# Performance work log

Hardware: AMD Instinct MI355X
Metric: run time of the kernel (lower is better)

## Reference

```python
import jax, jax.numpy as jnp
import numpy as np

B, S, D, H, DH = 4, 2048, 1024, 16, 64
INIT_STD = 0.02
IGNORE = -100000.0


def setup_inputs() -> dict:
    key = jax.random.key(0)
    ks = jax.random.split(key, 5)
    x = jax.random.normal(ks[0], (B, S, D), dtype=jnp.float32)
    W_Q = INIT_STD * jax.random.normal(ks[1], (H, D, DH), dtype=jnp.float32)
    W_K = INIT_STD * jax.random.normal(ks[2], (H, D, DH), dtype=jnp.float32)
    W_V = INIT_STD * jax.random.normal(ks[3], (H, D, DH), dtype=jnp.float32)
    W_O = INIT_STD * jax.random.normal(ks[4], (H, DH, D), dtype=jnp.float32)
    b_Q = jnp.zeros((H, DH), dtype=jnp.float32)
    b_K = jnp.zeros((H, DH), dtype=jnp.float32)
    b_V = jnp.zeros((H, DH), dtype=jnp.float32)
    b_O = jnp.zeros((D,), dtype=jnp.float32)
    return {"x": x, "W_Q": W_Q, "b_Q": b_Q, "W_K": W_K, "b_K": b_K,
            "W_V": W_V, "b_V": b_V, "W_O": W_O, "b_O": b_O}


def reference(x, W_Q, b_Q, W_K, b_K, W_V, b_V, W_O, b_O):
    # x: (B, S, D); projections -> (B, S, H, DH)
    Q = jnp.einsum('bqd,hde->bqhe', x, W_Q) + b_Q
    K = jnp.einsum('bkd,hde->bkhe', x, W_K) + b_K
    V = jnp.einsum('bkd,hde->bkhe', x, W_V) + b_V
    d_head = Q.shape[-1]
    # scores: (B, H, Sq, Sk)
    scores = jnp.einsum('bqhe,bkhe->bhqk', Q, K) / np.sqrt(d_head).astype(np.float32)
    s = scores.shape[-1]
    causal = jnp.triu(jnp.ones((s, s), dtype=bool), k=1)
    scores = jnp.where(causal, jnp.float32(IGNORE), scores)
    A = jax.nn.softmax(scores, axis=-1)
    z = jnp.einsum('bhqk,bkhe->bqhe', A, V)
    # output projection: sum over heads + bias
    attn_out = jnp.einsum('bqhe,hed->bqd', z, W_O) + b_O
    return attn_out
```

## Files before the change

kernel.cpp:

```cpp
#include <hip/hip_runtime.h>


#define B_ 4
#define S_ 2048
#define D_ 1024
#define H_ 16
#define DH_ 64

typedef unsigned short ushort_t;
typedef __attribute__((ext_vector_type(4))) short short4v;
typedef __attribute__((ext_vector_type(8))) short short8v;
typedef __attribute__((ext_vector_type(4))) float floatx4;
typedef __attribute__((ext_vector_type(4))) unsigned short ushort4v;

static __device__ __forceinline__ ushort_t f2bf(float f) {
    union { float f; unsigned u; } v; v.f = f;
    unsigned r = v.u + 0x7fffu + ((v.u >> 16) & 1u);
    return (ushort_t)(r >> 16);
}

static __device__ __forceinline__ float fast_exp2(float x) {
#if __has_builtin(__builtin_amdgcn_exp2f)
    return __builtin_amdgcn_exp2f(x);
#else
    return exp2f(x);
#endif
}

static __device__ __forceinline__ unsigned pack_bf16_tr(float lo, float hi) {
    union { float f; unsigned u; } a, b;
    a.f = lo; b.f = hi;
    return __builtin_amdgcn_perm(b.u, a.u, 0x07060302u);
}

static __device__ __forceinline__ void g2lds16(const void* g, void* l) {
    __builtin_amdgcn_global_load_lds(
        (__attribute__((address_space(1))) void*)(unsigned long long)(size_t)g,
        (__attribute__((address_space(3))) void*)(unsigned int)(size_t)l,
        16, 0, 0);
}

__global__ void convert_x_kernel(const float* __restrict__ x, ushort_t* __restrict__ xb) {
    int i = (blockIdx.x * 256 + threadIdx.x) * 4;
    float4 v = *(const float4*)&x[i];
    ushort4v o;
    o[0] = f2bf(v.x); o[1] = f2bf(v.y); o[2] = f2bf(v.z); o[3] = f2bf(v.w);
    *(ushort4v*)&xb[i] = o;
}

__global__ void transpose_nk_kernel(const float* __restrict__ s0, const float* __restrict__ s1,
                                    const float* __restrict__ s2, ushort_t* __restrict__ dst,
                                    int mode) {
    __shared__ float tile[32][33];
    int z = blockIdx.z;
    const float* src;
    ushort_t* d;
    int C;
    if (mode == 0) {
        src = (z < 16 ? s0 : (z < 32 ? s1 : s2)) + (size_t)(z & 15) * 65536;
        d = dst + (size_t)z * 65536;
        C = 64;
    } else {
        src = s0 + (size_t)z * 65536;
        d = dst + (size_t)z * 64;
        C = 1024;
    }
    int r0 = blockIdx.x * 32, c0 = blockIdx.y * 32;
    int tx = threadIdx.x, ty = threadIdx.y;
#pragma unroll
    for (int i = 0; i < 4; ++i)
        tile[ty + i * 8][tx] = src[(size_t)(r0 + ty + i * 8) * C + c0 + tx];
    __syncthreads();
#pragma unroll
    for (int i = 0; i < 4; ++i)
        d[(size_t)(c0 + ty + i * 8) * 1024 + r0 + tx] = f2bf(tile[tx][ty + i * 8]);
}

__global__ __launch_bounds__(256) void gemm_qkv(const ushort_t* __restrict__ A,
                                                const ushort_t* __restrict__ Wt,
                                                const float* __restrict__ bq,
                                                const float* __restrict__ bk,
                                                const float* __restrict__ bv,
                                                ushort_t* __restrict__ Qw,
                                                ushort_t* __restrict__ Kw,
                                                ushort_t* __restrict__ Vw) {
    __shared__ ushort_t sA[128 * 64];
    __shared__ ushort_t sB[128 * 64];
    const int tid = threadIdx.x;
    const int lane = tid & 63, w = tid >> 6;
    const int lq = lane & 15, quad = lane >> 4;
    const int wm = w >> 1, wn = w & 1;
    const int m0 = blockIdx.y * 128, n0 = blockIdx.x * 128;
    const int mat = blockIdx.x >> 3;

    floatx4 acc[4][4] = {};

    for (int k0 = 0; k0 < 1024; k0 += 64) {
        __syncthreads();
#pragma unroll
        for (int p = 0; p < 4; ++p) {
            int rr = w * 32 + p * 8 + (lane >> 3);
            int cc = (lane & 7) ^ (rr & 7);
            g2lds16(&A[(size_t)(m0 + rr) * 1024 + k0 + cc * 8], &sA[(w * 32 + p * 8) * 64]);
            g2lds16(&Wt[(size_t)(n0 + rr) * 1024 + k0 + cc * 8], &sB[(w * 32 + p * 8) * 64]);
        }
        __syncthreads();
#pragma unroll
        for (int ks = 0; ks < 2; ++ks) {
            short8v af[4], bfr[4];
#pragma unroll
            for (int t = 0; t < 4; ++t) {
                int ma = wm * 64 + t * 16 + lq;
                af[t] = *(const short8v*)&sA[ma * 64 + ((((ks << 2) | quad) ^ (ma & 7)) << 3)];
                int nb = wn * 64 + t * 16 + lq;
                bfr[t] = *(const short8v*)&sB[nb * 64 + ((((ks << 2) | quad) ^ (nb & 7)) << 3)];
            }
#pragma unroll
            for (int mt = 0; mt < 4; ++mt)
#pragma unroll
                for (int nt = 0; nt < 4; ++nt)
                    acc[mt][nt] = __builtin_amdgcn_mfma_f32_16x16x32_bf16(af[mt], bfr[nt], acc[mt][nt], 0, 0, 0);
        }
    }

    const float* bias = mat == 0 ? bq : (mat == 1 ? bk : bv);
    float bias_v[4];
#pragma unroll
    for (int nt = 0; nt < 4; ++nt) bias_v[nt] = bias[(n0 & 1023) + wn * 64 + nt * 16 + lq];

#pragma unroll
    for (int mt = 0; mt < 4; ++mt) {
#pragma unroll
        for (int nt = 0; nt < 4; ++nt) {
            int row0 = m0 + wm * 64 + mt * 16 + quad * 4;
            int col = (n0 & 1023) + wn * 64 + nt * 16 + lq;
            int h = col >> 6, e = col & 63;
            if (mat == 2) {
                int b = row0 >> 11, s = row0 & 2047;
                ushort4v pk;
#pragma unroll
                for (int rg = 0; rg < 4; ++rg) pk[rg] = f2bf(acc[mt][nt][rg] + bias_v[nt]);
                *(ushort4v*)&Vw[((size_t)((b << 4) | h) * 64 + e) * 2048 + s] = pk;
            } else {
                ushort_t* Du = mat == 0 ? Qw : Kw;
#pragma unroll
                for (int rg = 0; rg < 4; ++rg) {
                    int row = row0 + rg;
                    int b = row >> 11, s = row & 2047;
                    float v = acc[mt][nt][rg] + bias_v[nt];
                    if (mat == 0) v *= 0.18033688011112042f;
                    Du[((size_t)((b << 4) | h) * 2048 + s) * 64 + e] = f2bf(v);
                }
            }
        }
    }
}

#define VROW 132
__global__ __launch_bounds__(256) void attn_kernel(const ushort_t* __restrict__ Q,
                                                   const ushort_t* __restrict__ Kg,
                                                   const ushort_t* __restrict__ Vt,
                                                   ushort_t* __restrict__ Z) {
    __shared__ ushort_t sK[2][128 * 64];
    __shared__ ushort_t sV[64 * VROW];
    const int tid = threadIdx.x;
    const int lane = tid & 63, w = tid >> 6;
    const int lq = lane & 15, quad = lane >> 4;
    const int bh = blockIdx.y;
    const int b = bh >> 4, h = bh & 15;
    const ushort_t* Qp = Q + (size_t)bh * S_ * DH_;
    const ushort_t* Kp = Kg + (size_t)bh * S_ * DH_;
    const ushort_t* Vp = Vt + (size_t)bh * DH_ * S_;

    const int kbase0 = lq * 64 + ((quad ^ (lq & 7)) << 3);
    const int kbase1 = lq * 64 + (((4 | quad) ^ (lq & 7)) << 3);
    const int vbase = lq * VROW + quad * 4;
    const int vr = w * 16 + (lane >> 2);
    const int vc = (lane & 3) * 32;

    const floatx4 fzero = {0.f, 0.f, 0.f, 0.f};

    auto stageK = [&](int kt, int bs) __attribute__((always_inline)) {
        ushort_t* dK = sK[bs];
#pragma unroll
        for (int p = 0; p < 4; ++p) {
            int rrk = w * 32 + p * 8 + (lane >> 3);
            int ck = (lane & 7) ^ (rrk & 7);
            g2lds16(&Kp[(size_t)(kt * 128 + rrk) * 64 + ck * 8], &dK[(w * 32 + p * 8) * 64]);
        }
    };
    auto loadV = [&](int kt, short8v* vr4) __attribute__((always_inline)) {
        const ushort_t* src = &Vp[(size_t)vr * 2048 + kt * 128 + vc];
#pragma unroll
        for (int j = 0; j < 4; ++j) vr4[j] = *(const short8v*)&src[j * 8];
    };
    auto writeV = [&](const short8v* vr4) __attribute__((always_inline)) {
        ushort_t* dst = &sV[vr * VROW + vc];
#pragma unroll
        for (int j = 0; j < 4; ++j) *(short8v*)&dst[j * 8] = vr4[j];
    };

    for (int pass = 0; pass < 2; ++pass) {
        const int qt = pass == 0 ? (int)blockIdx.x : 15 - (int)blockIdx.x;
        const int q0 = qt * 128;

        short8v qf[2][2];
#pragma unroll
        for (int qi = 0; qi < 2; ++qi)
#pragma unroll
            for (int ks = 0; ks < 2; ++ks)
                qf[qi][ks] = *(const short8v*)&Qp[(size_t)(q0 + w * 32 + qi * 16 + lq) * DH_ + ks * 32 + quad * 8];

        float l_i[2] = {0.f, 0.f};
        floatx4 o[2][4] = {};
        short8v vreg[4];

        stageK(0, 0);
        loadV(0, vreg);

        for (int kt = 0; kt <= qt; ++kt) {
            const bool diag = (kt == qt);
            const ushort_t* cK = sK[kt & 1];

            __syncthreads();
            writeV(vreg);
            if (kt < qt) {
                stageK(kt + 1, (kt + 1) & 1);
                loadV(kt + 1, vreg);
            }

            floatx4 st[8][2];
#pragma unroll
            for (int si = 0; si < 8; ++si) {
                short8v a0 = *(const short8v*)&cK[kbase0 + si * 1024];
                short8v a1 = *(const short8v*)&cK[kbase1 + si * 1024];
#pragma unroll
                for (int qi = 0; qi < 2; ++qi) {
                    st[si][qi] = __builtin_amdgcn_mfma_f32_16x16x32_bf16(a0, qf[qi][0], fzero, 0, 0, 0);
                    st[si][qi] = __builtin_amdgcn_mfma_f32_16x16x32_bf16(a1, qf[qi][1], st[si][qi], 0, 0, 0);
                }
            }

            short4v pf[8][2];
#pragma unroll
            for (int qi = 0; qi < 2; ++qi) {
                const int qg = q0 + w * 32 + qi * 16 + lq;
                float lsum = 0.f;
#pragma unroll
                for (int si = 0; si < 8; ++si) {
                    float p[4];
#pragma unroll
                    for (int rg = 0; rg < 4; ++rg) {
                        float v = st[si][qi][rg];
                        if (diag) {
                            int sg = kt * 128 + si * 16 + quad * 4 + rg;
                            if (sg > qg) v = -1e30f;
                        }
                        p[rg] = fast_exp2(v);
                        lsum += p[rg];
                    }
                    union { unsigned u[2]; short4v v4; } pk;
                    pk.u[0] = pack_bf16_tr(p[0], p[1]);
                    pk.u[1] = pack_bf16_tr(p[2], p[3]);
                    pf[si][qi] = pk.v4;
                }
                l_i[qi] += lsum;
            }

            __syncthreads();

#pragma unroll
            for (int ksp = 0; ksp < 8; ++ksp) {
#pragma unroll
                for (int et = 0; et < 4; ++et) {
                    short4v vf = *(const short4v*)&sV[vbase + et * (16 * VROW) + ksp * 16];
#pragma unroll
                    for (int qi = 0; qi < 2; ++qi)
                        o[qi][et] = __builtin_amdgcn_mfma_f32_16x16x16bf16_1k(pf[ksp][qi], vf, o[qi][et], 0, 0, 0);
                }
            }
        }

#pragma unroll
        for (int qi = 0; qi < 2; ++qi) {
            float lf = l_i[qi];
            lf += __shfl_xor(lf, 16);
            lf += __shfl_xor(lf, 32);
            float linv[4];
#pragma unroll
            for (int rg = 0; rg < 4; ++rg) linv[rg] = 1.0f / __shfl(lf, quad * 4 + rg);
#pragma unroll
            for (int et = 0; et < 4; ++et) {
#pragma unroll
                for (int rg = 0; rg < 4; ++rg) {
                    int qg = q0 + w * 32 + qi * 16 + quad * 4 + rg;
                    int e = et * 16 + lq;
                    Z[((size_t)(b * S_ + qg) * H_ + h) * DH_ + e] = f2bf(o[qi][et][rg] * linv[rg]);
                }
            }
        }
    }
}

__global__ __launch_bounds__(256) void gemm_o(const ushort_t* __restrict__ A,
                                              const ushort_t* __restrict__ Bt,
                                              const float* __restrict__ bias,
                                              float* __restrict__ Dst) {
    __shared__ ushort_t sA[128 * 64];
    __shared__ ushort_t sB[128 * 64];
    const int tid = threadIdx.x;
    const int lane = tid & 63, w = tid >> 6;
    const int lq = lane & 15, quad = lane >> 4;
    const int wm = w >> 1, wn = w & 1;
    const int m0 = blockIdx.y * 128, n0 = blockIdx.x * 128;

    floatx4 acc[4][4] = {};

    for (int k0 = 0; k0 < 1024; k0 += 64) {
        __syncthreads();
#pragma unroll
        for (int p = 0; p < 4; ++p) {
            int rr = w * 32 + p * 8 + (lane >> 3);
            int cc = (lane & 7) ^ (rr & 7);
            g2lds16(&A[(size_t)(m0 + rr) * 1024 + k0 + cc * 8], &sA[(w * 32 + p * 8) * 64]);
            g2lds16(&Bt[(size_t)(n0 + rr) * 1024 + k0 + cc * 8], &sB[(w * 32 + p * 8) * 64]);
        }
        __syncthreads();
#pragma unroll
        for (int ks = 0; ks < 2; ++ks) {
            short8v af[4], bfr[4];
#pragma unroll
            for (int t = 0; t < 4; ++t) {
                int ma = wm * 64 + t * 16 + lq;
                af[t] = *(const short8v*)&sA[ma * 64 + ((((ks << 2) | quad) ^ (ma & 7)) << 3)];
                int nb = wn * 64 + t * 16 + lq;
                bfr[t] = *(const short8v*)&sB[nb * 64 + ((((ks << 2) | quad) ^ (nb & 7)) << 3)];
            }
#pragma unroll
            for (int mt = 0; mt < 4; ++mt)
#pragma unroll
                for (int nt = 0; nt < 4; ++nt)
                    acc[mt][nt] = __builtin_amdgcn_mfma_f32_16x16x32_bf16(af[mt], bfr[nt], acc[mt][nt], 0, 0, 0);
        }
    }

    float bias_v[4];
#pragma unroll
    for (int nt = 0; nt < 4; ++nt) bias_v[nt] = bias[n0 + wn * 64 + nt * 16 + lq];

#pragma unroll
    for (int mt = 0; mt < 4; ++mt) {
#pragma unroll
        for (int nt = 0; nt < 4; ++nt) {
            int row0 = m0 + wm * 64 + mt * 16 + quad * 4;
            int col = n0 + wn * 64 + nt * 16 + lq;
#pragma unroll
            for (int rg = 0; rg < 4; ++rg)
                Dst[(size_t)(row0 + rg) * 1024 + col] = acc[mt][nt][rg] + bias_v[nt];
        }
    }
}

extern "C" void kernel_launch(void* const* d_in, const int* in_sizes, int n_in,
                              void* d_out, int out_size, void* d_ws, size_t ws_size,
                              hipStream_t stream) {
    const float* x  = (const float*)d_in[0];
    const float* wq = (const float*)d_in[1];
    const float* bq = (const float*)d_in[2];
    const float* wk = (const float*)d_in[3];
    const float* bk = (const float*)d_in[4];
    const float* wv = (const float*)d_in[5];
    const float* bv = (const float*)d_in[6];
    const float* wo = (const float*)d_in[7];
    const float* bo = (const float*)d_in[8];

    char* ws = (char*)d_ws;
    size_t off = 0;
    ushort_t* xb  = (ushort_t*)(ws + off); off += (size_t)8192 * 1024 * 2;
    ushort_t* wt  = (ushort_t*)(ws + off); off += (size_t)3 * 1024 * 1024 * 2;
    ushort_t* wot = (ushort_t*)(ws + off); off += (size_t)1024 * 1024 * 2;
    ushort_t* Qw  = (ushort_t*)(ws + off); off += (size_t)8192 * 1024 * 2;
    ushort_t* Kw  = (ushort_t*)(ws + off); off += (size_t)8192 * 1024 * 2;
    ushort_t* Vw  = (ushort_t*)(ws + off); off += (size_t)8192 * 1024 * 2;
    ushort_t* Zw  = (ushort_t*)(ws + off); off += (size_t)8192 * 1024 * 2;

    convert_x_kernel<<<8192, 256, 0, stream>>>(x, xb);
    transpose_nk_kernel<<<dim3(32, 2, 48), dim3(32, 8), 0, stream>>>(wq, wk, wv, wt, 0);
    transpose_nk_kernel<<<dim3(2, 32, 16), dim3(32, 8), 0, stream>>>(wo, nullptr, nullptr, wot, 1);
    gemm_qkv<<<dim3(24, 64), 256, 0, stream>>>(xb, wt, bq, bk, bv, Qw, Kw, Vw);
    attn_kernel<<<dim3(8, 64), 256, 0, stream>>>(Qw, Kw, Vw, Zw);
    gemm_o<<<dim3(8, 64), 256, 0, stream>>>(Zw, wot, bo, (float*)d_out);
}
```

Measured before the change: 268.5 us.

## Merge prep kernels into one launch and swap grid axes for block ordering

Folds the x conversion and both weight-transpose kernels into a single prep launch, removing two kernel launches. It swaps the grid dimensions in the QKV GEMM, attention and output GEMM so that consecutive blocks walk along M (or batch-head) rather than N, which changes L2 reuse of the weight and activation tiles across concurrently scheduled blocks. It also changes the V LDS row padding from 132 to 140 to alter the bank-conflict pattern. The reordering could help or hurt cache locality, and the merged prep kernel adds a branch on block index.

```diff
diff --git a/kernel.cpp b/kernel.cpp
--- a/kernel.cpp
+++ b/kernel.cpp
@@ -40,33 +40,39 @@
         16, 0, 0);
 }
 
-__global__ void convert_x_kernel(const float* __restrict__ x, ushort_t* __restrict__ xb) {
-    int i = (blockIdx.x * 256 + threadIdx.x) * 4;
-    float4 v = *(const float4*)&x[i];
-    ushort4v o;
-    o[0] = f2bf(v.x); o[1] = f2bf(v.y); o[2] = f2bf(v.z); o[3] = f2bf(v.w);
-    *(ushort4v*)&xb[i] = o;
-}
-
-__global__ void transpose_nk_kernel(const float* __restrict__ s0, const float* __restrict__ s1,
-                                    const float* __restrict__ s2, ushort_t* __restrict__ dst,
-                                    int mode) {
+__global__ void prep_kernel(const float* __restrict__ x,
+                            const float* __restrict__ wq, const float* __restrict__ wk,
+                            const float* __restrict__ wv, const float* __restrict__ wo,
+                            ushort_t* __restrict__ xb, ushort_t* __restrict__ wt,
+                            ushort_t* __restrict__ wot) {
     __shared__ float tile[32][33];
-    int z = blockIdx.z;
+    int bid = blockIdx.x;
+    int tid = threadIdx.x;
+    if (bid < 8192) {
+        int i = (bid * 256 + tid) * 4;
+        float4 v = *(const float4*)&x[i];
+        ushort4v o;
+        o[0] = f2bf(v.x); o[1] = f2bf(v.y); o[2] = f2bf(v.z); o[3] = f2bf(v.w);
+        *(ushort4v*)&xb[i] = o;
+        return;
+    }
     const float* src;
     ushort_t* d;
-    int C;
-    if (mode == 0) {
-        src = (z < 16 ? s0 : (z < 32 ? s1 : s2)) + (size_t)(z & 15) * 65536;
-        d = dst + (size_t)z * 65536;
-        C = 64;
+    int C, r0, c0;
+    if (bid < 11264) {
+        int t = bid - 8192;
+        int z = t / 64, r = t % 64;
+        src = (z < 16 ? wq : (z < 32 ? wk : wv)) + (size_t)(z & 15) * 65536;
+        d = wt + (size_t)z * 65536;
+        C = 64; r0 = (r >> 1) * 32; c0 = (r & 1) * 32;
     } else {
-        src = s0 + (size_t)z * 65536;
-        d = dst + (size_t)z * 64;
-        C = 1024;
-    }
-    int r0 = blockIdx.x * 32, c0 = blockIdx.y * 32;
-    int tx = threadIdx.x, ty = threadIdx.y;
+        int t = bid - 11264;
+        int z = t / 64, r = t % 64;
+        src = wo + (size_t)z * 65536;
+        d = wot + (size_t)z * 64;
+        C = 1024; r0 = (r & 1) * 32; c0 = (r >> 1) * 32;
+    }
+    int tx = tid & 31, ty = tid >> 5;
 #pragma unroll
     for (int i = 0; i < 4; ++i)
         tile[ty + i * 8][tx] = src[(size_t)(r0 + ty + i * 8) * C + c0 + tx];
@@ -90,8 +96,8 @@
     const int lane = tid & 63, w = tid >> 6;
     const int lq = lane & 15, quad = lane >> 4;
     const int wm = w >> 1, wn = w & 1;
-    const int m0 = blockIdx.y * 128, n0 = blockIdx.x * 128;
-    const int mat = blockIdx.x >> 3;
+    const int m0 = blockIdx.x * 128, n0 = blockIdx.y * 128;
+    const int mat = blockIdx.y >> 3;
 
     floatx4 acc[4][4] = {};
 
@@ -156,7 +162,7 @@
     }
 }
 
-#define VROW 132
+#define VROW 140
 __global__ __launch_bounds__(256) void attn_kernel(const ushort_t* __restrict__ Q,
                                                    const ushort_t* __restrict__ Kg,
                                                    const ushort_t* __restrict__ Vt,
@@ -166,7 +172,7 @@
     const int tid = threadIdx.x;
     const int lane = tid & 63, w = tid >> 6;
     const int lq = lane & 15, quad = lane >> 4;
-    const int bh = blockIdx.y;
+    const int bh = blockIdx.x;
     const int b = bh >> 4, h = bh & 15;
     const ushort_t* Qp = Q + (size_t)bh * S_ * DH_;
     const ushort_t* Kp = Kg + (size_t)bh * S_ * DH_;
@@ -201,7 +207,7 @@
     };
 
     for (int pass = 0; pass < 2; ++pass) {
-        const int qt = pass == 0 ? (int)blockIdx.x : 15 - (int)blockIdx.x;
+        const int qt = pass == 0 ? (int)blockIdx.y : 15 - (int)blockIdx.y;
         const int q0 = qt * 128;
 
         short8v qf[2][2];
@@ -312,7 +318,7 @@
     const int lane = tid & 63, w = tid >> 6;
     const int lq = lane & 15, quad = lane >> 4;
     const int wm = w >> 1, wn = w & 1;
-    const int m0 = blockIdx.y * 128, n0 = blockIdx.x * 128;
+    const int m0 = blockIdx.x * 128, n0 = blockIdx.y * 128;
 
     floatx4 acc[4][4] = {};
 
@@ -384,10 +390,8 @@
     ushort_t* Vw  = (ushort_t*)(ws + off); off += (size_t)8192 * 1024 * 2;
     ushort_t* Zw  = (ushort_t*)(ws + off); off += (size_t)8192 * 1024 * 2;
 
-    convert_x_kernel<<<8192, 256, 0, stream>>>(x, xb);
-    transpose_nk_kernel<<<dim3(32, 2, 48), dim3(32, 8), 0, stream>>>(wq, wk, wv, wt, 0);
-    transpose_nk_kernel<<<dim3(2, 32, 16), dim3(32, 8), 0, stream>>>(wo, nullptr, nullptr, wot, 1);
-    gemm_qkv<<<dim3(24, 64), 256, 0, stream>>>(xb, wt, bq, bk, bv, Qw, Kw, Vw);
-    attn_kernel<<<dim3(8, 64), 256, 0, stream>>>(Qw, Kw, Vw, Zw);
-    gemm_o<<<dim3(8, 64), 256, 0, stream>>>(Zw, wot, bo, (float*)d_out);
-}
+    prep_kernel<<<12288, 256, 0, stream>>>(x, wq, wk, wv, wo, xb, wt, wot);
+    gemm_qkv<<<dim3(64, 24), 256, 0, stream>>>(xb, wt, bq, bk, bv, Qw, Kw, Vw);
+    attn_kernel<<<dim3(64, 8), 256, 0, stream>>>(Qw, Kw, Vw, Zw);
+    gemm_o<<<dim3(64, 8), 256, 0, stream>>>(Zw, wot, bo, (float*)d_out);
+}
```

New measurement: 252.8 us. -5.9%, faster.
